# Performance work log

Measured on AMD Instinct MI355X. Metric: run time of the kernel, lower is better.

The kernel has to match this reference:

```python
import jax, jax.numpy as jnp
import numpy as np

N = 50000      # num nodes
E = 400000     # num directed edges
IN = 128       # in_channels
H = 256        # hidden_channels
OUT = 128      # out_channels
LN_EPS = 1e-5


def setup_inputs() -> dict:
    key = jax.random.key(0)
    ks = jax.random.split(key, 12)
    x = jax.random.normal(ks[0], (N, IN), jnp.float32)
    edge_index = jax.random.randint(ks[1], (2, E), 0, N, jnp.int32)

    def lin(k, fi, fo):
        return jax.random.normal(k, (fi, fo), jnp.float32) / jnp.sqrt(jnp.float32(fi))

    return {
        "x": x,
        "edge_index": edge_index,
        "W1": lin(ks[2], IN, H),  "b1": jnp.zeros((H,), jnp.float32),
        "W2": lin(ks[3], H, H),   "b2": jnp.zeros((H,), jnp.float32),
        "W3": lin(ks[4], H, H),   "b3": jnp.zeros((H,), jnp.float32),
        "W4": lin(ks[5], H, OUT), "b4": jnp.zeros((OUT,), jnp.float32),
        "g1": jnp.ones((H,), jnp.float32),   "be1": jnp.zeros((H,), jnp.float32),
        "g2": jnp.ones((H,), jnp.float32),   "be2": jnp.zeros((H,), jnp.float32),
        "g3": jnp.ones((H,), jnp.float32),   "be3": jnp.zeros((H,), jnp.float32),
        "g4": jnp.ones((OUT,), jnp.float32), "be4": jnp.zeros((OUT,), jnp.float32),
    }


def layer_norm(h, g, b):
    m = jnp.mean(h, axis=-1, keepdims=True)
    v = jnp.mean(jnp.square(h - m), axis=-1, keepdims=True)
    return (h - m) * jax.lax.rsqrt(v + LN_EPS) * g + b


def gcn_conv(h, W, b, src, dst, dinv):
    # PyG GCNConv: add self-loops, norm = deg^-1/2[src] * deg^-1/2[dst]
    h = h @ W                                             # [N, F_out]
    norm = (dinv[src] * dinv[dst])[:, None]               # [E, 1]
    msg = h[src] * norm                                   # [E, F_out] irregular gather
    agg = jax.ops.segment_sum(msg, dst, num_segments=N)   # scatter-add
    agg = agg + h * jnp.square(dinv)[:, None]             # self-loop term
    return agg + b


def reference(x, edge_index, W1, b1, W2, b2, W3, b3, W4, b4,
              g1, be1, g2, be2, g3, be3, g4, be4):
    src, dst = edge_index[0], edge_index[1]
    # degree (incl. self-loop) from destination index, as in PyG gcn_norm
    deg = jax.ops.segment_sum(jnp.ones((E,), jnp.float32), dst, num_segments=N) + 1.0
    dinv = jax.lax.rsqrt(deg)

    h = gcn_conv(x, W1, b1, src, dst, dinv)
    h = jax.nn.relu(layer_norm(h, g1, be1))   # dropout = identity (eval)
    h = gcn_conv(h, W2, b2, src, dst, dinv)
    h = jax.nn.relu(layer_norm(h, g2, be2))
    h = gcn_conv(h, W3, b3, src, dst, dinv)
    h = jax.nn.relu(layer_norm(h, g3, be3))
    h = gcn_conv(h, W4, b4, src, dst, dinv)
    h = layer_norm(h, g4, be4)
    return h
```

## Files before the change

### kernel.cpp

```cpp
#include <hip/hip_runtime.h>

#define NN 50000
#define NEDGE 400000
#define MPAD 50048
#define NB 196
constexpr float LN_EPS = 1e-5f;

typedef __attribute__((ext_vector_type(8))) short bf16x8;
typedef __attribute__((ext_vector_type(4))) float f32x4;
typedef __attribute__((ext_vector_type(8))) unsigned short ushort8v;

__device__ __forceinline__ unsigned short f2bf(float f) {
  unsigned int u = __float_as_uint(f);
  u += 0x7FFFu + ((u >> 16) & 1u);
  return (unsigned short)(u >> 16);
}
__device__ __forceinline__ float bf2f(unsigned short u) {
  return __uint_as_float(((unsigned int)u) << 16);
}

__global__ __launch_bounds__(256) void k_prep(
    const float* __restrict__ W1, const float* __restrict__ W2,
    const float* __restrict__ W3, const float* __restrict__ W4,
    unsigned short* __restrict__ Wt1, unsigned short* __restrict__ Wt2,
    unsigned short* __restrict__ Wt3, unsigned short* __restrict__ Wt4,
    const float* __restrict__ x, unsigned short* __restrict__ xB,
    int* __restrict__ cnt) {
  const int b = blockIdx.x;
  const int n = threadIdx.x;
  if (b < 128) {
    Wt1[(size_t)n * 128 + b] = f2bf(W1[(size_t)b * 256 + n]);
  } else if (b < 384) {
    const int k = b - 128;
    Wt2[(size_t)n * 256 + k] = f2bf(W2[(size_t)k * 256 + n]);
  } else if (b < 640) {
    const int k = b - 384;
    Wt3[(size_t)n * 256 + k] = f2bf(W3[(size_t)k * 256 + n]);
  } else if (b < 896) {
    const int k = b - 640;
    if (n < 128) Wt4[(size_t)n * 256 + k] = f2bf(W4[(size_t)k * 128 + n]);
  } else if (b < 7146) {
    const int i = (b - 896) * 256 + n;
    float4 v = reinterpret_cast<const float4*>(x)[i];
    ushort4 o; o.x = f2bf(v.x); o.y = f2bf(v.y); o.z = f2bf(v.z); o.w = f2bf(v.w);
    reinterpret_cast<ushort4*>(xB)[i] = o;
  } else {
    const int i = (b - 7146) * 256 + n;
    if (i < NN) cnt[i] = 0;
  }
}

__global__ void k_count(const int* __restrict__ dst, int* __restrict__ cnt) {
  int e = blockIdx.x * blockDim.x + threadIdx.x;
  if (e < NEDGE) atomicAdd(&cnt[dst[e]], 1);
}

__global__ __launch_bounds__(256) void k_bsum(const int* __restrict__ cnt,
                                              int* __restrict__ bsum,
                                              float* __restrict__ dinv) {
  const int i = blockIdx.x * 256 + threadIdx.x;
  int v = 0;
  if (i < NN) {
    v = cnt[i];
    dinv[i] = rsqrtf((float)v + 1.0f);
  }
  int s = v;
#pragma unroll
  for (int off = 32; off > 0; off >>= 1) s += __shfl_xor(s, off);
  __shared__ int wsum[4];
  if ((threadIdx.x & 63) == 0) wsum[threadIdx.x >> 6] = s;
  __syncthreads();
  if (threadIdx.x == 0) bsum[blockIdx.x] = wsum[0] + wsum[1] + wsum[2] + wsum[3];
}

__global__ __launch_bounds__(256) void k_bapply(const int* __restrict__ cnt,
                                                const int* __restrict__ bsum,
                                                int* __restrict__ rowptr,
                                                int* __restrict__ cursor) {
  __shared__ int sOff[NB];
  __shared__ int wsum[4], woff[4];
  const int t = threadIdx.x;
  const int lane = t & 63, wid = t >> 6;

  {
    int v = (t < NB) ? bsum[t] : 0;
    int inc = v;
    for (int off = 1; off < 64; off <<= 1) {
      int y = __shfl_up(inc, off);
      if (lane >= off) inc += y;
    }
    if (lane == 63) wsum[wid] = inc;
    __syncthreads();
    if (t == 0) {
      int run = 0;
      for (int w = 0; w < 4; ++w) { woff[w] = run; run += wsum[w]; }
    }
    __syncthreads();
    if (t < NB) sOff[t] = woff[wid] + inc - v;
  }
  __syncthreads();

  const int i = blockIdx.x * 256 + t;
  int v = (i < NN) ? cnt[i] : 0;
  int inc = v;
  for (int off = 1; off < 64; off <<= 1) {
    int y = __shfl_up(inc, off);
    if (lane >= off) inc += y;
  }
  if (lane == 63) wsum[wid] = inc;
  __syncthreads();
  if (t == 0) {
    int run = 0;
    for (int w = 0; w < 4; ++w) { woff[w] = run; run += wsum[w]; }
  }
  __syncthreads();
  if (i < NN) {
    const int rp = sOff[blockIdx.x] + woff[wid] + inc - v;
    rowptr[i] = rp;
    cursor[i] = rp;
  }
  if (blockIdx.x == 0 && t == 0) rowptr[NN] = NEDGE;
}

__global__ void k_fill(const int* __restrict__ src, const int* __restrict__ dst,
                       const float* __restrict__ dinv, int* __restrict__ cursor,
                       int2* __restrict__ eidx2) {
  int e = blockIdx.x * blockDim.x + threadIdx.x;
  if (e >= NEDGE) return;
  const int d = dst[e];
  const int s = src[e];
  const int p = atomicAdd(&cursor[d], 1);
  eidx2[p] = make_int2(s, __float_as_int(dinv[s] * dinv[d]));
}

template<int F, int NPW, int MODE>
__global__ __launch_bounds__(256) void k_gather(
    const int* __restrict__ rowptr, const int2* __restrict__ eidx2,
    const float* __restrict__ dinv, const unsigned short* __restrict__ h,
    void* __restrict__ outv, const float* __restrict__ bias,
    const float* __restrict__ gamma, const float* __restrict__ beta) {
  constexpr int LPN = 64 / NPW;
  static_assert(F / LPN == 8, "16B per lane");
  const int tid = threadIdx.x;
  const int lane = tid & 63;
  const int sub = lane / LPN;
  const int slane = lane % LPN;
  const int n = blockIdx.x * (4 * NPW) + (tid >> 6) * NPW + sub;
  const bool valid = n < NN;

  int e = 0, end = 0;
  float dn = 0.f;
  if (valid) {
    dn = dinv[n];
    e = rowptr[n];
    end = rowptr[n + 1];
  }

  float acc[8];
  ushort8v r0 = (ushort8v)0, r1 = (ushort8v)0, r2 = (ushort8v)0, r3 = (ushort8v)0;
  if (valid) r0 = *reinterpret_cast<const ushort8v*>(h + (size_t)n * F + slane * 8);
  const float sw = dn * dn;
#pragma unroll
  for (int j = 0; j < 8; ++j) acc[j] = bf2f(r0[j]) * sw;
  r0 = (ushort8v)0;

  while (__ballot(e < end)) {
    float w0 = 0.f, w1 = 0.f, w2 = 0.f, w3 = 0.f;
    if (e < end) {
      const int2 p = eidx2[e];
      w0 = __int_as_float(p.y);
      r0 = *reinterpret_cast<const ushort8v*>(h + (size_t)p.x * F + slane * 8);
    }
    if (e + 1 < end) {
      const int2 p = eidx2[e + 1];
      w1 = __int_as_float(p.y);
      r1 = *reinterpret_cast<const ushort8v*>(h + (size_t)p.x * F + slane * 8);
    }
    if (e + 2 < end) {
      const int2 p = eidx2[e + 2];
      w2 = __int_as_float(p.y);
      r2 = *reinterpret_cast<const ushort8v*>(h + (size_t)p.x * F + slane * 8);
    }
    if (e + 3 < end) {
      const int2 p = eidx2[e + 3];
      w3 = __int_as_float(p.y);
      r3 = *reinterpret_cast<const ushort8v*>(h + (size_t)p.x * F + slane * 8);
    }
#pragma unroll
    for (int j = 0; j < 8; ++j)
      acc[j] += w0 * bf2f(r0[j]) + w1 * bf2f(r1[j]) + w2 * bf2f(r2[j]) + w3 * bf2f(r3[j]);
    e += 4;
  }

  if (!valid) return;

  if constexpr (MODE == 0) {
    ushort8v o;
#pragma unroll
    for (int j = 0; j < 8; ++j) o[j] = f2bf(acc[j]);
    *reinterpret_cast<ushort8v*>((unsigned short*)outv + (size_t)n * F + slane * 8) = o;
  } else {
    const float4 b0 = *reinterpret_cast<const float4*>(bias + slane * 8);
    const float4 b1 = *reinterpret_cast<const float4*>(bias + slane * 8 + 4);
    acc[0] += b0.x; acc[1] += b0.y; acc[2] += b0.z; acc[3] += b0.w;
    acc[4] += b1.x; acc[5] += b1.y; acc[6] += b1.z; acc[7] += b1.w;
    float s = 0.f, q = 0.f;
#pragma unroll
    for (int j = 0; j < 8; ++j) { s += acc[j]; q = fmaf(acc[j], acc[j], q); }
#pragma unroll
    for (int off = 1; off < 16; off <<= 1) {
      s += __shfl_xor(s, off);
      q += __shfl_xor(q, off);
    }
    const float mean = s * (1.0f / 128.0f);
    const float var = q * (1.0f / 128.0f) - mean * mean;
    const float inv = rsqrtf(var + LN_EPS);
    const float4 g0 = *reinterpret_cast<const float4*>(gamma + slane * 8);
    const float4 g1 = *reinterpret_cast<const float4*>(gamma + slane * 8 + 4);
    const float4 e0 = *reinterpret_cast<const float4*>(beta + slane * 8);
    const float4 e1 = *reinterpret_cast<const float4*>(beta + slane * 8 + 4);
    float4 o0, o1;
    o0.x = (acc[0] - mean) * inv * g0.x + e0.x;
    o0.y = (acc[1] - mean) * inv * g0.y + e0.y;
    o0.z = (acc[2] - mean) * inv * g0.z + e0.z;
    o0.w = (acc[3] - mean) * inv * g0.w + e0.w;
    o1.x = (acc[4] - mean) * inv * g1.x + e1.x;
    o1.y = (acc[5] - mean) * inv * g1.y + e1.y;
    o1.z = (acc[6] - mean) * inv * g1.z + e1.z;
    o1.w = (acc[7] - mean) * inv * g1.w + e1.w;
    float* out = (float*)outv + (size_t)n * 128 + slane * 8;
    *reinterpret_cast<float4*>(out) = o0;
    *reinterpret_cast<float4*>(out + 4) = o1;
  }
}

template<int K, int N, bool LNFUSE>
__global__ __launch_bounds__(256) void k_mgemm(const unsigned short* __restrict__ A,
                                               const unsigned short* __restrict__ Bt,
                                               const float* __restrict__ bias,
                                               const float* __restrict__ gamma,
                                               const float* __restrict__ beta,
                                               unsigned short* __restrict__ out) {
  constexpr int NT = N / 64;
  constexpr int KS = K / 32;
  __shared__ __align__(16) unsigned short As[64 * K];

  const int tid = threadIdx.x;
  const int lane = tid & 63;
  const int w = tid >> 6;
  const int m0 = blockIdx.x * 64;

#pragma unroll
  for (int i = 0; i < KS; ++i) {
    const int o = (i * 256 + tid) * 16;
    const int row = o / (2 * K);
    const int inb = o % (2 * K);
    uint4 val = *reinterpret_cast<const uint4*>(
        (const char*)A + (size_t)(m0 + row) * (2 * K) + inb);
    const int dsto = o ^ ((row & 7) << 4);
    *reinterpret_cast<uint4*>((char*)As + dsto) = val;
  }
  __syncthreads();

  f32x4 acc[4][NT];
#pragma unroll
  for (int mt = 0; mt < 4; ++mt)
#pragma unroll
    for (int nt = 0; nt < NT; ++nt) acc[mt][nt] = (f32x4){0.f, 0.f, 0.f, 0.f};

  const int nw0 = w * (N / 4);
  const int arow = lane & 15;
  const int kgrp = (lane >> 4) * 8;

  for (int ks = 0; ks < KS; ++ks) {
    bf16x8 af[4];
#pragma unroll
    for (int mt = 0; mt < 4; ++mt) {
      const int r = mt * 16 + arow;
      int boff = (r * K + ks * 32 + kgrp) * 2;
      boff ^= (r & 7) << 4;
      af[mt] = *reinterpret_cast<const bf16x8*>((const char*)As + boff);
    }
    bf16x8 bfr[NT];
#pragma unroll
    for (int nt = 0; nt < NT; ++nt) {
      const int n = nw0 + nt * 16 + arow;
      bfr[nt] = *reinterpret_cast<const bf16x8*>(Bt + (size_t)n * K + ks * 32 + kgrp);
    }
#pragma unroll
    for (int mt = 0; mt < 4; ++mt)
#pragma unroll
      for (int nt = 0; nt < NT; ++nt)
        acc[mt][nt] = __builtin_amdgcn_mfma_f32_16x16x32_bf16(af[mt], bfr[nt], acc[mt][nt], 0, 0, 0);
  }

  const int g = lane >> 4;
  const int cl = lane & 15;

  if constexpr (LNFUSE) {
    float gv[NT], bev[NT];
#pragma unroll
    for (int nt = 0; nt < NT; ++nt) {
      const int c = nw0 + nt * 16 + cl;
      const float bv = bias[c];
      gv[nt] = gamma[c];
      bev[nt] = beta[c];
#pragma unroll
      for (int mt = 0; mt < 4; ++mt)
#pragma unroll
        for (int reg = 0; reg < 4; ++reg) acc[mt][nt][reg] += bv;
    }
    __shared__ float sS[4][64];
    __shared__ float sQ[4][64];
    float ps[4][4], pq[4][4];
#pragma unroll
    for (int mt = 0; mt < 4; ++mt) {
#pragma unroll
      for (int reg = 0; reg < 4; ++reg) {
        float s = 0.f, q = 0.f;
#pragma unroll
        for (int nt = 0; nt < NT; ++nt) {
          const float v = acc[mt][nt][reg];
          s += v; q = fmaf(v, v, q);
        }
#pragma unroll
        for (int off = 1; off < 16; off <<= 1) {
          s += __shfl_xor(s, off);
          q += __shfl_xor(q, off);
        }
        ps[mt][reg] = s; pq[mt][reg] = q;
      }
    }
    if (cl == 0) {
#pragma unroll
      for (int mt = 0; mt < 4; ++mt)
#pragma unroll
        for (int reg = 0; reg < 4; ++reg) {
          sS[w][mt * 16 + g * 4 + reg] = ps[mt][reg];
          sQ[w][mt * 16 + g * 4 + reg] = pq[mt][reg];
        }
    }
    __syncthreads();
#pragma unroll
    for (int mt = 0; mt < 4; ++mt) {
#pragma unroll
      for (int reg = 0; reg < 4; ++reg) {
        const int rr = mt * 16 + g * 4 + reg;
        const int r = m0 + rr;
        const float S = sS[0][rr] + sS[1][rr] + sS[2][rr] + sS[3][rr];
        const float Q = sQ[0][rr] + sQ[1][rr] + sQ[2][rr] + sQ[3][rr];
        const float mean = S * (1.0f / N);
        const float var = Q * (1.0f / N) - mean * mean;
        const float inv = rsqrtf(var + LN_EPS);
        if (r < NN) {
#pragma unroll
          for (int nt = 0; nt < NT; ++nt) {
            const int c = nw0 + nt * 16 + cl;
            const float o = fmaxf((acc[mt][nt][reg] - mean) * inv * gv[nt] + bev[nt], 0.f);
            out[(size_t)r * N + c] = f2bf(o);
          }
        }
      }
    }
  } else {
#pragma unroll
    for (int mt = 0; mt < 4; ++mt) {
#pragma unroll
      for (int nt = 0; nt < NT; ++nt) {
        const int c = nw0 + nt * 16 + cl;
#pragma unroll
        for (int reg = 0; reg < 4; ++reg) {
          const int r = m0 + mt * 16 + g * 4 + reg;
          if (r < NN) out[(size_t)r * N + c] = f2bf(acc[mt][nt][reg]);
        }
      }
    }
  }
}

extern "C" void kernel_launch(void* const* d_in, const int* in_sizes, int n_in,
                              void* d_out, int out_size, void* d_ws, size_t ws_size,
                              hipStream_t stream) {
  const float* x   = (const float*)d_in[0];
  const int*   ei  = (const int*)d_in[1];
  const float* W1  = (const float*)d_in[2];
  const float* b1  = (const float*)d_in[3];
  const float* W2  = (const float*)d_in[4];
  const float* b2  = (const float*)d_in[5];
  const float* W3  = (const float*)d_in[6];
  const float* b3  = (const float*)d_in[7];
  const float* W4  = (const float*)d_in[8];
  const float* b4  = (const float*)d_in[9];
  const float* g1  = (const float*)d_in[10];
  const float* be1 = (const float*)d_in[11];
  const float* g2  = (const float*)d_in[12];
  const float* be2 = (const float*)d_in[13];
  const float* g3  = (const float*)d_in[14];
  const float* be3 = (const float*)d_in[15];
  const float* g4  = (const float*)d_in[16];
  const float* be4 = (const float*)d_in[17];

  const int* src = ei;
  const int* dst = ei + NEDGE;

  char* ws = (char*)d_ws;
  int*   cnt    = (int*)(ws + 0);
  int*   cursor = (int*)(ws + 204800);
  int*   rowptr = (int*)(ws + 409600);
  float* dinv   = (float*)(ws + 614400);
  int*   bsum   = (int*)(ws + 819200);
  int2*  eidx2  = (int2*)(ws + 827392);
  unsigned short* Wt1 = (unsigned short*)(ws + 4030464);
  unsigned short* Wt2 = (unsigned short*)(ws + 4096000);
  unsigned short* Wt3 = (unsigned short*)(ws + 4227072);
  unsigned short* Wt4 = (unsigned short*)(ws + 4358144);
  unsigned short* xB  = (unsigned short*)(ws + 4423680);
  unsigned short* aggB = (unsigned short*)(ws + 17235968);
  unsigned short* hB   = (unsigned short*)(ws + 42860544);
  unsigned short* t4B  = (unsigned short*)(ws + 68485120);
  float* out = (float*)d_out;

  const int MB = (NN + 63) / 64;

  k_prep<<<7342, 256, 0, stream>>>(W1, W2, W3, W4, Wt1, Wt2, Wt3, Wt4, x, xB, cnt);
  k_count<<<(NEDGE + 255) / 256, 256, 0, stream>>>(dst, cnt);
  k_bsum<<<NB, 256, 0, stream>>>(cnt, bsum, dinv);
  k_bapply<<<NB, 256, 0, stream>>>(cnt, bsum, rowptr, cursor);
  k_fill<<<(NEDGE + 255) / 256, 256, 0, stream>>>(src, dst, dinv, cursor, eidx2);

  k_gather<128, 4, 0><<<(NN + 15) / 16, 256, 0, stream>>>(rowptr, eidx2, dinv, xB, aggB, nullptr, nullptr, nullptr);
  k_mgemm<128, 256, true><<<MB, 256, 0, stream>>>(aggB, Wt1, b1, g1, be1, hB);

  k_gather<256, 2, 0><<<(NN + 7) / 8, 256, 0, stream>>>(rowptr, eidx2, dinv, hB, aggB, nullptr, nullptr, nullptr);
  k_mgemm<256, 256, true><<<MB, 256, 0, stream>>>(aggB, Wt2, b2, g2, be2, hB);

  k_gather<256, 2, 0><<<(NN + 7) / 8, 256, 0, stream>>>(rowptr, eidx2, dinv, hB, aggB, nullptr, nullptr, nullptr);
  k_mgemm<256, 256, true><<<MB, 256, 0, stream>>>(aggB, Wt3, b3, g3, be3, hB);

  k_mgemm<256, 128, false><<<MB, 256, 0, stream>>>(hB, Wt4, nullptr, nullptr, nullptr, t4B);
  k_gather<128, 4, 1><<<(NN + 15) / 16, 256, 0, stream>>>(rowptr, eidx2, dinv, t4B, out, b4, g4, be4);
}
```

Baseline: 285.3 us.

## Fuse neighbor gather into GEMM+LayerNorm kernel via shared-memory A tile

```diff
diff --git a/kernel.cpp b/kernel.cpp
--- a/kernel.cpp
+++ b/kernel.cpp
@@ -133,113 +133,182 @@
   eidx2[p] = make_int2(s, __float_as_int(dinv[s] * dinv[d]));
 }
 
-template<int F, int NPW, int MODE>
-__global__ __launch_bounds__(256) void k_gather(
+template<int K, int N>
+__global__ __launch_bounds__(256) void k_gg(
     const int* __restrict__ rowptr, const int2* __restrict__ eidx2,
-    const float* __restrict__ dinv, const unsigned short* __restrict__ h,
-    void* __restrict__ outv, const float* __restrict__ bias,
-    const float* __restrict__ gamma, const float* __restrict__ beta) {
-  constexpr int LPN = 64 / NPW;
-  static_assert(F / LPN == 8, "16B per lane");
+    const float* __restrict__ dinv, const unsigned short* __restrict__ hIn,
+    const unsigned short* __restrict__ Bt, const float* __restrict__ bias,
+    const float* __restrict__ gamma, const float* __restrict__ beta,
+    unsigned short* __restrict__ out) {
+  constexpr int LPN = K / 8;
+  constexpr int NPW = 64 / LPN;
+  constexpr int NT = N / 64;
+  constexpr int KS = K / 32;
+  __shared__ __align__(16) unsigned short As[64 * K];
+
   const int tid = threadIdx.x;
   const int lane = tid & 63;
+  const int w = tid >> 6;
+  const int m0 = blockIdx.x * 64;
   const int sub = lane / LPN;
   const int slane = lane % LPN;
-  const int n = blockIdx.x * (4 * NPW) + (tid >> 6) * NPW + sub;
-  const bool valid = n < NN;
-
-  int e = 0, end = 0;
-  float dn = 0.f;
-  if (valid) {
-    dn = dinv[n];
-    e = rowptr[n];
-    end = rowptr[n + 1];
-  }
-
-  float acc[8];
-  ushort8v r0 = (ushort8v)0, r1 = (ushort8v)0, r2 = (ushort8v)0, r3 = (ushort8v)0;
-  if (valid) r0 = *reinterpret_cast<const ushort8v*>(h + (size_t)n * F + slane * 8);
-  const float sw = dn * dn;
-#pragma unroll
-  for (int j = 0; j < 8; ++j) acc[j] = bf2f(r0[j]) * sw;
-  r0 = (ushort8v)0;
-
-  while (__ballot(e < end)) {
-    float w0 = 0.f, w1 = 0.f, w2 = 0.f, w3 = 0.f;
-    if (e < end) {
-      const int2 p = eidx2[e];
-      w0 = __int_as_float(p.y);
-      r0 = *reinterpret_cast<const ushort8v*>(h + (size_t)p.x * F + slane * 8);
-    }
-    if (e + 1 < end) {
-      const int2 p = eidx2[e + 1];
-      w1 = __int_as_float(p.y);
-      r1 = *reinterpret_cast<const ushort8v*>(h + (size_t)p.x * F + slane * 8);
-    }
-    if (e + 2 < end) {
-      const int2 p = eidx2[e + 2];
-      w2 = __int_as_float(p.y);
-      r2 = *reinterpret_cast<const ushort8v*>(h + (size_t)p.x * F + slane * 8);
-    }
-    if (e + 3 < end) {
-      const int2 p = eidx2[e + 3];
-      w3 = __int_as_float(p.y);
-      r3 = *reinterpret_cast<const ushort8v*>(h + (size_t)p.x * F + slane * 8);
-    }
-#pragma unroll
-    for (int j = 0; j < 8; ++j)
-      acc[j] += w0 * bf2f(r0[j]) + w1 * bf2f(r1[j]) + w2 * bf2f(r2[j]) + w3 * bf2f(r3[j]);
-    e += 4;
-  }
-
-  if (!valid) return;
-
-  if constexpr (MODE == 0) {
-    ushort8v o;
-#pragma unroll
-    for (int j = 0; j < 8; ++j) o[j] = f2bf(acc[j]);
-    *reinterpret_cast<ushort8v*>((unsigned short*)outv + (size_t)n * F + slane * 8) = o;
-  } else {
-    const float4 b0 = *reinterpret_cast<const float4*>(bias + slane * 8);
-    const float4 b1 = *reinterpret_cast<const float4*>(bias + slane * 8 + 4);
-    acc[0] += b0.x; acc[1] += b0.y; acc[2] += b0.z; acc[3] += b0.w;
-    acc[4] += b1.x; acc[5] += b1.y; acc[6] += b1.z; acc[7] += b1.w;
-    float s = 0.f, q = 0.f;
-#pragma unroll
-    for (int j = 0; j < 8; ++j) { s += acc[j]; q = fmaf(acc[j], acc[j], q); }
-#pragma unroll
-    for (int off = 1; off < 16; off <<= 1) {
-      s += __shfl_xor(s, off);
-      q += __shfl_xor(q, off);
-    }
-    const float mean = s * (1.0f / 128.0f);
-    const float var = q * (1.0f / 128.0f) - mean * mean;
-    const float inv = rsqrtf(var + LN_EPS);
-    const float4 g0 = *reinterpret_cast<const float4*>(gamma + slane * 8);
-    const float4 g1 = *reinterpret_cast<const float4*>(gamma + slane * 8 + 4);
-    const float4 e0 = *reinterpret_cast<const float4*>(beta + slane * 8);
-    const float4 e1 = *reinterpret_cast<const float4*>(beta + slane * 8 + 4);
-    float4 o0, o1;
-    o0.x = (acc[0] - mean) * inv * g0.x + e0.x;
-    o0.y = (acc[1] - mean) * inv * g0.y + e0.y;
-    o0.z = (acc[2] - mean) * inv * g0.z + e0.z;
-    o0.w = (acc[3] - mean) * inv * g0.w + e0.w;
-    o1.x = (acc[4] - mean) * inv * g1.x + e1.x;
-    o1.y = (acc[5] - mean) * inv * g1.y + e1.y;
-    o1.z = (acc[6] - mean) * inv * g1.z + e1.z;
-    o1.w = (acc[7] - mean) * inv * g1.w + e1.w;
-    float* out = (float*)outv + (size_t)n * 128 + slane * 8;
-    *reinterpret_cast<float4*>(out) = o0;
-    *reinterpret_cast<float4*>(out + 4) = o1;
-  }
-}
-
-template<int K, int N, bool LNFUSE>
+
+  for (int it = 0; it < 16 / NPW; ++it) {
+    const int rr = w * 16 + it * NPW + sub;
+    const int n = m0 + rr;
+    const bool valid = n < NN;
+    int e = 0, end = 0;
+    float dn = 0.f;
+    if (valid) { dn = dinv[n]; e = rowptr[n]; end = rowptr[n + 1]; }
+    float acc[8];
+    ushort8v r0 = (ushort8v)0, r1 = (ushort8v)0, r2 = (ushort8v)0, r3 = (ushort8v)0;
+    if (valid) r0 = *reinterpret_cast<const ushort8v*>(hIn + (size_t)n * K + slane * 8);
+    const float sw = dn * dn;
+#pragma unroll
+    for (int j = 0; j < 8; ++j) acc[j] = bf2f(r0[j]) * sw;
+    r0 = (ushort8v)0;
+
+    while (__ballot(e < end)) {
+      float w0 = 0.f, w1 = 0.f, w2 = 0.f, w3 = 0.f;
+      if (e < end) {
+        const int2 p = eidx2[e];
+        w0 = __int_as_float(p.y);
+        r0 = *reinterpret_cast<const ushort8v*>(hIn + (size_t)p.x * K + slane * 8);
+      }
+      if (e + 1 < end) {
+        const int2 p = eidx2[e + 1];
+        w1 = __int_as_float(p.y);
+        r1 = *reinterpret_cast<const ushort8v*>(hIn + (size_t)p.x * K + slane * 8);
+      }
+      if (e + 2 < end) {
+        const int2 p = eidx2[e + 2];
+        w2 = __int_as_float(p.y);
+        r2 = *reinterpret_cast<const ushort8v*>(hIn + (size_t)p.x * K + slane * 8);
+      }
+      if (e + 3 < end) {
+        const int2 p = eidx2[e + 3];
+        w3 = __int_as_float(p.y);
+        r3 = *reinterpret_cast<const ushort8v*>(hIn + (size_t)p.x * K + slane * 8);
+      }
+#pragma unroll
+      for (int j = 0; j < 8; ++j)
+        acc[j] += w0 * bf2f(r0[j]) + w1 * bf2f(r1[j]) + w2 * bf2f(r2[j]) + w3 * bf2f(r3[j]);
+      e += 4;
+    }
+
+    ushort8v ob;
+#pragma unroll
+    for (int j = 0; j < 8; ++j) ob[j] = f2bf(acc[j]);
+    int boff = (rr * K + slane * 8) * 2;
+    boff ^= (rr & 7) << 4;
+    *reinterpret_cast<ushort8v*>((char*)As + boff) = ob;
+  }
+  __syncthreads();
+
+  f32x4 acc[4][NT];
+#pragma unroll
+  for (int mt = 0; mt < 4; ++mt)
+#pragma unroll
+    for (int nt = 0; nt < NT; ++nt) acc[mt][nt] = (f32x4){0.f, 0.f, 0.f, 0.f};
+
+  const int nw0 = w * (N / 4);
+  const int arow = lane & 15;
+  const int kgrp = (lane >> 4) * 8;
+
+  for (int ks = 0; ks < KS; ++ks) {
+    bf16x8 af[4];
+#pragma unroll
+    for (int mt = 0; mt < 4; ++mt) {
+      const int r = mt * 16 + arow;
+      int boff = (r * K + ks * 32 + kgrp) * 2;
+      boff ^= (r & 7) << 4;
+      af[mt] = *reinterpret_cast<const bf16x8*>((const char*)As + boff);
+    }
+    bf16x8 bfr[NT];
+#pragma unroll
+    for (int nt = 0; nt < NT; ++nt) {
+      const int n = nw0 + nt * 16 + arow;
+      bfr[nt] = *reinterpret_cast<const bf16x8*>(Bt + (size_t)n * K + ks * 32 + kgrp);
+    }
+#pragma unroll
+    for (int mt = 0; mt < 4; ++mt)
+#pragma unroll
+      for (int nt = 0; nt < NT; ++nt)
+        acc[mt][nt] = __builtin_amdgcn_mfma_f32_16x16x32_bf16(af[mt], bfr[nt], acc[mt][nt], 0, 0, 0);
+  }
+
+  const int g = lane >> 4;
+  const int cl = lane & 15;
+
+  float gv[NT], bev[NT];
+#pragma unroll
+  for (int nt = 0; nt < NT; ++nt) {
+    const int c = nw0 + nt * 16 + cl;
+    const float bv = bias[c];
+    gv[nt] = gamma[c];
+    bev[nt] = beta[c];
+#pragma unroll
+    for (int mt = 0; mt < 4; ++mt)
+#pragma unroll
+      for (int reg = 0; reg < 4; ++reg) acc[mt][nt][reg] += bv;
+  }
+  __shared__ float sS[4][64];
+  __shared__ float sQ[4][64];
+  float ps[4][4], pq[4][4];
+#pragma unroll
+  for (int mt = 0; mt < 4; ++mt) {
+#pragma unroll
+    for (int reg = 0; reg < 4; ++reg) {
+      float s = 0.f, q = 0.f;
+#pragma unroll
+      for (int nt = 0; nt < NT; ++nt) {
+        const float v = acc[mt][nt][reg];
+        s += v; q = fmaf(v, v, q);
+      }
+#pragma unroll
+      for (int off = 1; off < 16; off <<= 1) {
+        s += __shfl_xor(s, off);
+        q += __shfl_xor(q, off);
+      }
+      ps[mt][reg] = s; pq[mt][reg] = q;
+    }
+  }
+  if (cl == 0) {
+#pragma unroll
+    for (int mt = 0; mt < 4; ++mt)
+#pragma unroll
+      for (int reg = 0; reg < 4; ++reg) {
+        sS[w][mt * 16 + g * 4 + reg] = ps[mt][reg];
+        sQ[w][mt * 16 + g * 4 + reg] = pq[mt][reg];
+      }
+  }
+  __syncthreads();
+#pragma unroll
+  for (int mt = 0; mt < 4; ++mt) {
+#pragma unroll
+    for (int reg = 0; reg < 4; ++reg) {
+      const int rr = mt * 16 + g * 4 + reg;
+      const int r = m0 + rr;
+      const float S = sS[0][rr] + sS[1][rr] + sS[2][rr] + sS[3][rr];
+      const float Q = sQ[0][rr] + sQ[1][rr] + sQ[2][rr] + sQ[3][rr];
+      const float mean = S * (1.0f / N);
+      const float var = Q * (1.0f / N) - mean * mean;
+      const float inv = rsqrtf(var + LN_EPS);
+      if (r < NN) {
+#pragma unroll
+        for (int nt = 0; nt < NT; ++nt) {
+          const int c = nw0 + nt * 16 + cl;
+          const float o = fmaxf((acc[mt][nt][reg] - mean) * inv * gv[nt] + bev[nt], 0.f);
+          out[(size_t)r * N + c] = f2bf(o);
+        }
+      }
+    }
+  }
+}
+
+template<int K, int N>
 __global__ __launch_bounds__(256) void k_mgemm(const unsigned short* __restrict__ A,
                                                const unsigned short* __restrict__ Bt,
-                                               const float* __restrict__ bias,
-                                               const float* __restrict__ gamma,
-                                               const float* __restrict__ beta,
                                                unsigned short* __restrict__ out) {
   constexpr int NT = N / 64;
   constexpr int KS = K / 32;
@@ -296,86 +365,110 @@
 
   const int g = lane >> 4;
   const int cl = lane & 15;
-
-  if constexpr (LNFUSE) {
-    float gv[NT], bev[NT];
+#pragma unroll
+  for (int mt = 0; mt < 4; ++mt) {
 #pragma unroll
     for (int nt = 0; nt < NT; ++nt) {
       const int c = nw0 + nt * 16 + cl;
-      const float bv = bias[c];
-      gv[nt] = gamma[c];
-      bev[nt] = beta[c];
-#pragma unroll
-      for (int mt = 0; mt < 4; ++mt)
-#pragma unroll
-        for (int reg = 0; reg < 4; ++reg) acc[mt][nt][reg] += bv;
-    }
-    __shared__ float sS[4][64];
-    __shared__ float sQ[4][64];
-    float ps[4][4], pq[4][4];
-#pragma unroll
-    for (int mt = 0; mt < 4; ++mt) {
 #pragma unroll
       for (int reg = 0; reg < 4; ++reg) {
-        float s = 0.f, q = 0.f;
-#pragma unroll
-        for (int nt = 0; nt < NT; ++nt) {
-          const float v = acc[mt][nt][reg];
-          s += v; q = fmaf(v, v, q);
-        }
-#pragma unroll
-        for (int off = 1; off < 16; off <<= 1) {
-          s += __shfl_xor(s, off);
-          q += __shfl_xor(q, off);
-        }
-        ps[mt][reg] = s; pq[mt][reg] = q;
-      }
-    }
-    if (cl == 0) {
-#pragma unroll
-      for (int mt = 0; mt < 4; ++mt)
-#pragma unroll
-        for (int reg = 0; reg < 4; ++reg) {
-          sS[w][mt * 16 + g * 4 + reg] = ps[mt][reg];
-          sQ[w][mt * 16 + g * 4 + reg] = pq[mt][reg];
-        }
-    }
-    __syncthreads();
-#pragma unroll
-    for (int mt = 0; mt < 4; ++mt) {
-#pragma unroll
-      for (int reg = 0; reg < 4; ++reg) {
-        const int rr = mt * 16 + g * 4 + reg;
-        const int r = m0 + rr;
-        const float S = sS[0][rr] + sS[1][rr] + sS[2][rr] + sS[3][rr];
-        const float Q = sQ[0][rr] + sQ[1][rr] + sQ[2][rr] + sQ[3][rr];
-        const float mean = S * (1.0f / N);
-        const float var = Q * (1.0f / N) - mean * mean;
-        const float inv = rsqrtf(var + LN_EPS);
-        if (r < NN) {
-#pragma unroll
-          for (int nt = 0; nt < NT; ++nt) {
-            const int c = nw0 + nt * 16 + cl;
-            const float o = fmaxf((acc[mt][nt][reg] - mean) * inv * gv[nt] + bev[nt], 0.f);
-            out[(size_t)r * N + c] = f2bf(o);
-          }
-        }
-      }
-    }
-  } else {
-#pragma unroll
-    for (int mt = 0; mt < 4; ++mt) {
-#pragma unroll
-      for (int nt = 0; nt < NT; ++nt) {
-        const int c = nw0 + nt * 16 + cl;
-#pragma unroll
-        for (int reg = 0; reg < 4; ++reg) {
-          const int r = m0 + mt * 16 + g * 4 + reg;
-          if (r < NN) out[(size_t)r * N + c] = f2bf(acc[mt][nt][reg]);
-        }
-      }
-    }
-  }
+        const int r = m0 + mt * 16 + g * 4 + reg;
+        if (r < NN) out[(size_t)r * N + c] = f2bf(acc[mt][nt][reg]);
+      }
+    }
+  }
+}
+
+__global__ __launch_bounds__(256) void k_gather_final(
+    const int* __restrict__ rowptr, const int2* __restrict__ eidx2,
+    const float* __restrict__ dinv, const unsigned short* __restrict__ h,
+    float* __restrict__ outv, const float* __restrict__ bias,
+    const float* __restrict__ gamma, const float* __restrict__ beta) {
+  constexpr int F = 128, LPN = 16, NPW = 4;
+  const int tid = threadIdx.x;
+  const int lane = tid & 63;
+  const int sub = lane / LPN;
+  const int slane = lane % LPN;
+  const int n = blockIdx.x * (4 * NPW) + (tid >> 6) * NPW + sub;
+  const bool valid = n < NN;
+
+  int e = 0, end = 0;
+  float dn = 0.f;
+  if (valid) {
+    dn = dinv[n];
+    e = rowptr[n];
+    end = rowptr[n + 1];
+  }
+
+  float acc[8];
+  ushort8v r0 = (ushort8v)0, r1 = (ushort8v)0, r2 = (ushort8v)0, r3 = (ushort8v)0;
+  if (valid) r0 = *reinterpret_cast<const ushort8v*>(h + (size_t)n * F + slane * 8);
+  const float sw = dn * dn;
+#pragma unroll
+  for (int j = 0; j < 8; ++j) acc[j] = bf2f(r0[j]) * sw;
+  r0 = (ushort8v)0;
+
+  while (__ballot(e < end)) {
+    float w0 = 0.f, w1 = 0.f, w2 = 0.f, w3 = 0.f;
+    if (e < end) {
+      const int2 p = eidx2[e];
+      w0 = __int_as_float(p.y);
+      r0 = *reinterpret_cast<const ushort8v*>(h + (size_t)p.x * F + slane * 8);
+    }
+    if (e + 1 < end) {
+      const int2 p = eidx2[e + 1];
+      w1 = __int_as_float(p.y);
+      r1 = *reinterpret_cast<const ushort8v*>(h + (size_t)p.x * F + slane * 8);
+    }
+    if (e + 2 < end) {
+      const int2 p = eidx2[e + 2];
+      w2 = __int_as_float(p.y);
+      r2 = *reinterpret_cast<const ushort8v*>(h + (size_t)p.x * F + slane * 8);
+    }
+    if (e + 3 < end) {
+      const int2 p = eidx2[e + 3];
+      w3 = __int_as_float(p.y);
+      r3 = *reinterpret_cast<const ushort8v*>(h + (size_t)p.x * F + slane * 8);
+    }
+#pragma unroll
+    for (int j = 0; j < 8; ++j)
+      acc[j] += w0 * bf2f(r0[j]) + w1 * bf2f(r1[j]) + w2 * bf2f(r2[j]) + w3 * bf2f(r3[j]);
+    e += 4;
+  }
+
+  if (!valid) return;
+
+  const float4 b0 = *reinterpret_cast<const float4*>(bias + slane * 8);
+  const float4 b1 = *reinterpret_cast<const float4*>(bias + slane * 8 + 4);
+  acc[0] += b0.x; acc[1] += b0.y; acc[2] += b0.z; acc[3] += b0.w;
+  acc[4] += b1.x; acc[5] += b1.y; acc[6] += b1.z; acc[7] += b1.w;
+  float s = 0.f, q = 0.f;
+#pragma unroll
+  for (int j = 0; j < 8; ++j) { s += acc[j]; q = fmaf(acc[j], acc[j], q); }
+#pragma unroll
+  for (int off = 1; off < 16; off <<= 1) {
+    s += __shfl_xor(s, off);
+    q += __shfl_xor(q, off);
+  }
+  const float mean = s * (1.0f / 128.0f);
+  const float var = q * (1.0f / 128.0f) - mean * mean;
+  const float inv = rsqrtf(var + LN_EPS);
+  const float4 g0 = *reinterpret_cast<const float4*>(gamma + slane * 8);
+  const float4 g1 = *reinterpret_cast<const float4*>(gamma + slane * 8 + 4);
+  const float4 e0 = *reinterpret_cast<const float4*>(beta + slane * 8);
+  const float4 e1 = *reinterpret_cast<const float4*>(beta + slane * 8 + 4);
+  float4 o0, o1;
+  o0.x = (acc[0] - mean) * inv * g0.x + e0.x;
+  o0.y = (acc[1] - mean) * inv * g0.y + e0.y;
+  o0.z = (acc[2] - mean) * inv * g0.z + e0.z;
+  o0.w = (acc[3] - mean) * inv * g0.w + e0.w;
+  o1.x = (acc[4] - mean) * inv * g1.x + e1.x;
+  o1.y = (acc[5] - mean) * inv * g1.y + e1.y;
+  o1.z = (acc[6] - mean) * inv * g1.z + e1.z;
+  o1.w = (acc[7] - mean) * inv * g1.w + e1.w;
+  float* out = outv + (size_t)n * 128 + slane * 8;
+  *reinterpret_cast<float4*>(out) = o0;
+  *reinterpret_cast<float4*>(out + 4) = o1;
 }
 
 extern "C" void kernel_launch(void* const* d_in, const int* in_sizes, int n_in,
@@ -415,9 +508,9 @@
   unsigned short* Wt3 = (unsigned short*)(ws + 4227072);
   unsigned short* Wt4 = (unsigned short*)(ws + 4358144);
   unsigned short* xB  = (unsigned short*)(ws + 4423680);
-  unsigned short* aggB = (unsigned short*)(ws + 17235968);
-  unsigned short* hB   = (unsigned short*)(ws + 42860544);
-  unsigned short* t4B  = (unsigned short*)(ws + 68485120);
+  unsigned short* hA  = (unsigned short*)(ws + 17235968);
+  unsigned short* hB  = (unsigned short*)(ws + 42860544);
+  unsigned short* t4B = (unsigned short*)(ws + 68485120);
   float* out = (float*)d_out;
 
   const int MB = (NN + 63) / 64;
@@ -428,15 +521,10 @@
   k_bapply<<<NB, 256, 0, stream>>>(cnt, bsum, rowptr, cursor);
   k_fill<<<(NEDGE + 255) / 256, 256, 0, stream>>>(src, dst, dinv, cursor, eidx2);
 
-  k_gather<128, 4, 0><<<(NN + 15) / 16, 256, 0, stream>>>(rowptr, eidx2, dinv, xB, aggB, nullptr, nullptr, nullptr);
-  k_mgemm<128, 256, true><<<MB, 256, 0, stream>>>(aggB, Wt1, b1, g1, be1, hB);
-
-  k_gather<256, 2, 0><<<(NN + 7) / 8, 256, 0, stream>>>(rowptr, eidx2, dinv, hB, aggB, nullptr, nullptr, nullptr);
-  k_mgemm<256, 256, true><<<MB, 256, 0, stream>>>(aggB, Wt2, b2, g2, be2, hB);
-
-  k_gather<256, 2, 0><<<(NN + 7) / 8, 256, 0, stream>>>(rowptr, eidx2, dinv, hB, aggB, nullptr, nullptr, nullptr);
-  k_mgemm<256, 256, true><<<MB, 256, 0, stream>>>(aggB, Wt3, b3, g3, be3, hB);
-
-  k_mgemm<256, 128, false><<<MB, 256, 0, stream>>>(hB, Wt4, nullptr, nullptr, nullptr, t4B);
-  k_gather<128, 4, 1><<<(NN + 15) / 16, 256, 0, stream>>>(rowptr, eidx2, dinv, t4B, out, b4, g4, be4);
-}
+  k_gg<128, 256><<<MB, 256, 0, stream>>>(rowptr, eidx2, dinv, xB, Wt1, b1, g1, be1, hA);
+  k_gg<256, 256><<<MB, 256, 0, stream>>>(rowptr, eidx2, dinv, hA, Wt2, b2, g2, be2, hB);
+  k_gg<256, 256><<<MB, 256, 0, stream>>>(rowptr, eidx2, dinv, hB, Wt3, b3, g3, be3, hA);
+
+  k_mgemm<256, 128><<<MB, 256, 0, stream>>>(hA, Wt4, t4B);
+  k_gather_final<<<(NN + 15) / 16, 256, 0, stream>>>(rowptr, eidx2, dinv, t4B, out, b4, g4, be4);
+}
```

Measured after the change: 388.0 us. 1.36x slower.
